# Performance work log

Measured on AMD Instinct MI355X. Metric: run time of the kernel, lower is better.

## Reference

```python
import jax, jax.numpy as jnp
import numpy as np

IN_F = 4096
OUT_F = 4096

def setup_inputs() -> dict:
    key = jax.random.key(0)
    k1, k2 = jax.random.split(key)
    x = jax.random.normal(k1, (8, 2048, IN_F), dtype=jnp.float32)
    weight = jax.random.normal(k2, (OUT_F, IN_F), dtype=jnp.float32) * (1.0 / IN_F ** 0.5)
    bias = jnp.zeros((OUT_F,), dtype=jnp.float32)
    return {"x": x, "weight": weight, "bias": bias}

def reference(x, weight, bias):
    # absmean scale over the full weight matrix (BitNet b1.58)
    scale = jnp.maximum(jnp.mean(jnp.abs(weight)), 1e-8)
    w_quant = jnp.clip(jnp.round(weight / scale), -1.0, 1.0)  # ternary {-1,0,+1}
    # straight-through estimator: forward uses w_quant*scale, grad flows to weight
    w_ste = jax.lax.stop_gradient(w_quant * scale - weight) + weight
    # x: [b, s, in], w_ste: [out, in] -> [b, s, out]
    return jnp.einsum('bsi,oi->bso', x, w_ste) + bias
```

## Files before the change

kernel.cpp:

```cpp
#include <hip/hip_runtime.h>
#include <stdint.h>
#include <stddef.h>

#define M_DIM 16384
#define K_DIM 4096
#define N_DIM 4096

#define BM 128
#define BN 128
#define BK 32

#define WS_SUM_OFF   0
#define WS_PART_OFF  256
#define WS_X_OFF     16384
#define WS_XBYTES    ((size_t)M_DIM * K_DIM * 2)
#define WS_W_OFF     (WS_X_OFF + WS_XBYTES)
#define WS_WBYTES    ((size_t)N_DIM * K_DIM * 2)
#define WS_NEEDED    (WS_W_OFF + WS_WBYTES)

typedef __attribute__((ext_vector_type(8))) short short8;
typedef __attribute__((ext_vector_type(4))) float floatx4;

__device__ __forceinline__ unsigned short f2bf_rne(float f) {
  unsigned u = __builtin_bit_cast(unsigned, f);
  u += 0x7FFFu + ((u >> 16) & 1u);
  return (unsigned short)(u >> 16);
}

__device__ __forceinline__ float get_scale(const double* __restrict__ sum) {
  double m = *sum * (1.0 / 16777216.0);
  return (float)fmax(m, 1e-8);
}

__device__ __forceinline__ void gload16(const void* g, void* l) {
  __builtin_amdgcn_global_load_lds(
      (const __attribute__((address_space(1))) void*)g,
      (__attribute__((address_space(3))) void*)l,
      16, 0, 0);
}

__global__ void prep_kernel(const float* __restrict__ W, double* __restrict__ partials,
                            const float* __restrict__ X, unsigned short* __restrict__ XO) {
  if (blockIdx.x < 1024) {
    const int n4 = (N_DIM * K_DIM) / 4;
    const float4* W4 = (const float4*)W;
    float s = 0.f;
    const int stride = 1024 * blockDim.x;
    for (int i = blockIdx.x * blockDim.x + threadIdx.x; i < n4; i += stride) {
      float4 v = W4[i];
      s += fabsf(v.x) + fabsf(v.y) + fabsf(v.z) + fabsf(v.w);
    }
#pragma unroll
    for (int off = 32; off > 0; off >>= 1) s += __shfl_down(s, off);
    __shared__ double bsum[4];
    if ((threadIdx.x & 63) == 0) bsum[threadIdx.x >> 6] = (double)s;
    __syncthreads();
    if (threadIdx.x == 0)
      partials[blockIdx.x] = bsum[0] + bsum[1] + bsum[2] + bsum[3];
  } else {
    const int n4 = (M_DIM * K_DIM) / 4;
    const float4* X4 = (const float4*)X;
    ushort4* O4 = (ushort4*)XO;
    const int nblk = 3072;
    const int stride = nblk * blockDim.x;
    for (int i = (blockIdx.x - 1024) * blockDim.x + threadIdx.x; i < n4; i += stride) {
      float4 v = X4[i];
      ushort4 o;
      o.x = f2bf_rne(v.x); o.y = f2bf_rne(v.y); o.z = f2bf_rne(v.z); o.w = f2bf_rne(v.w);
      O4[i] = o;
    }
  }
}

__global__ void reduce2_kernel(const double* __restrict__ partials, double* __restrict__ sum) {
  double s = 0.0;
  for (int i = threadIdx.x; i < 1024; i += 256) s += partials[i];
#pragma unroll
  for (int off = 32; off > 0; off >>= 1) s += __shfl_down(s, off);
  __shared__ double wsum[4];
  if ((threadIdx.x & 63) == 0) wsum[threadIdx.x >> 6] = s;
  __syncthreads();
  if (threadIdx.x == 0) *sum = wsum[0] + wsum[1] + wsum[2] + wsum[3];
}

__global__ void quantw_kernel(const float* __restrict__ W, const double* __restrict__ sum,
                              unsigned short* __restrict__ T) {
  const int n4 = (N_DIM * K_DIM) / 4;
  const float s = get_scale(sum);
  const float4* W4 = (const float4*)W;
  ushort4* T4 = (ushort4*)T;
  const int stride = gridDim.x * blockDim.x;
  for (int i = blockIdx.x * blockDim.x + threadIdx.x; i < n4; i += stride) {
    float4 v = W4[i];
    float q0 = fminf(fmaxf(rintf(v.x / s), -1.f), 1.f);
    float q1 = fminf(fmaxf(rintf(v.y / s), -1.f), 1.f);
    float q2 = fminf(fmaxf(rintf(v.z / s), -1.f), 1.f);
    float q3 = fminf(fmaxf(rintf(v.w / s), -1.f), 1.f);
    ushort4 o;
    o.x = f2bf_rne(q0); o.y = f2bf_rne(q1); o.z = f2bf_rne(q2); o.w = f2bf_rne(q3);
    T4[i] = o;
  }
}

__global__ __launch_bounds__(256) void gemm_kernel(
    const unsigned short* __restrict__ A,
    const unsigned short* __restrict__ B,
    const float* __restrict__ bias,
    const double* __restrict__ sum,
    float* __restrict__ C) {
  __shared__ __align__(16) unsigned short sA[BM * BK];
  __shared__ __align__(16) unsigned short sB[BN * BK];

  const int tid = threadIdx.x;
  const int w = tid >> 6;
  const int l = tid & 63;
  const int wm = w & 1;
  const int wn = w >> 1;
  const int blockM = blockIdx.y * BM;
  const int blockN = blockIdx.x * BN;

  const int srow = w * 16 + (l >> 2);
  const int skc = ((l & 3) ^ ((l >> 3) & 3)) * 8;
  const unsigned short* pA0 = A + (size_t)(blockM + srow) * K_DIM + skc;
  const unsigned short* pA1 = pA0 + (size_t)64 * K_DIM;
  const unsigned short* pB0 = B + (size_t)(blockN + srow) * K_DIM + skc;
  const unsigned short* pB1 = pB0 + (size_t)64 * K_DIM;
  char* ldsA0 = (char*)sA + w * 1024;
  char* ldsA1 = (char*)sA + 4096 + w * 1024;
  char* ldsB0 = (char*)sB + w * 1024;
  char* ldsB1 = (char*)sB + 4096 + w * 1024;

  const int arow = wm * 64 + (l & 15);
  const int brow = wn * 64 + (l & 15);
  const int koff = (((l >> 4) ^ ((l >> 1) & 3))) * 8;

  floatx4 acc[4][4] = {};

  for (int kt = 0; kt < K_DIM / BK; ++kt) {
    __syncthreads();
    gload16(pA0, ldsA0);
    gload16(pA1, ldsA1);
    gload16(pB0, ldsB0);
    gload16(pB1, ldsB1);
    pA0 += BK; pA1 += BK; pB0 += BK; pB1 += BK;
    __syncthreads();

    short8 af[4], bf[4];
#pragma unroll
    for (int mi = 0; mi < 4; ++mi)
      af[mi] = *(const short8*)&sA[(arow + mi * 16) * BK + koff];
#pragma unroll
    for (int ni = 0; ni < 4; ++ni)
      bf[ni] = *(const short8*)&sB[(brow + ni * 16) * BK + koff];
#pragma unroll
    for (int mi = 0; mi < 4; ++mi)
#pragma unroll
      for (int ni = 0; ni < 4; ++ni)
        acc[mi][ni] = __builtin_amdgcn_mfma_f32_16x16x32_bf16(
            af[mi], bf[ni], acc[mi][ni], 0, 0, 0);
  }

  const float s = get_scale(sum);
  const int col16 = l & 15;
  const int rquad = (l >> 4) * 4;
#pragma unroll
  for (int mi = 0; mi < 4; ++mi) {
#pragma unroll
    for (int ni = 0; ni < 4; ++ni) {
      const int col = blockN + wn * 64 + ni * 16 + col16;
      const float bv = bias[col];
      const int row0 = blockM + wm * 64 + mi * 16 + rquad;
#pragma unroll
      for (int r = 0; r < 4; ++r) {
        C[(size_t)(row0 + r) * N_DIM + col] = acc[mi][ni][r] * s + bv;
      }
    }
  }
}

extern "C" void kernel_launch(void* const* d_in, const int* in_sizes, int n_in,
                              void* d_out, int out_size, void* d_ws, size_t ws_size,
                              hipStream_t stream) {
  const float* x = (const float*)d_in[0];
  const float* wt = (const float*)d_in[1];
  const float* bias = (const float*)d_in[2];
  float* out = (float*)d_out;

  if (ws_size < WS_NEEDED) return;

  double* sum = (double*)((char*)d_ws + WS_SUM_OFF);
  double* partials = (double*)((char*)d_ws + WS_PART_OFF);
  unsigned short* xb = (unsigned short*)((char*)d_ws + WS_X_OFF);
  unsigned short* wb = (unsigned short*)((char*)d_ws + WS_W_OFF);

  prep_kernel<<<4096, 256, 0, stream>>>(wt, partials, x, xb);
  reduce2_kernel<<<1, 256, 0, stream>>>(partials, sum);
  quantw_kernel<<<1024, 256, 0, stream>>>(wt, sum, wb);
  dim3 grid(N_DIM / BN, M_DIM / BM);
  gemm_kernel<<<grid, 256, 0, stream>>>(xb, wb, bias, sum, out);
}
```

Measured before the change: 1.083 ms.

## Rewrite GEMM as 256x256x64 double-buffered pipelined kernel with interleaved staging

Replaces the 128x128x32 single-buffered GEMM with a 512-thread 256x256x64 tile kernel. Its 128KB LDS is split into two ping-pong buffers, and global-to-LDS loads for future k-tiles are interleaved between MFMA quads, using explicit barriers, waitcnt and setprio. It also remaps block IDs for L2 locality and changes the LDS XOR swizzle. The aim is to hide global load latency and raise arithmetic intensity per LDS byte, at the cost of heavy register and LDS use and fragile hand-tuned synchronization.

```diff
diff --git a/kernel.cpp b/kernel.cpp
--- a/kernel.cpp
+++ b/kernel.cpp
@@ -6,9 +6,9 @@
 #define K_DIM 4096
 #define N_DIM 4096
 
-#define BM 128
-#define BN 128
-#define BK 32
+#define BM 256
+#define BN 256
+#define BK 64
 
 #define WS_SUM_OFF   0
 #define WS_PART_OFF  256
@@ -102,78 +102,175 @@
   }
 }
 
-__global__ __launch_bounds__(256) void gemm_kernel(
+__device__ __forceinline__ void stage64(const unsigned short* __restrict__ src,
+                                        int gRow0, int kBase, char* ldsSlab) {
+  const int t = threadIdx.x;
+  const int r = t >> 3;
+  const int g = (t & 7) ^ (r & 7);
+  gload16(src + (size_t)(gRow0 + r) * K_DIM + kBase + (g << 3),
+          ldsSlab + ((t >> 6) << 10));
+}
+
+template <int Q>
+__device__ __forceinline__ void mfma_quad(floatx4 (&acc)[8][4],
+                                          const short8 (&F)[2][2],
+                                          const short8 (&bfr)[4][2]) {
+#pragma unroll
+  for (int j = 0; j < 2; ++j) {
+#pragma unroll
+    for (int ni = 0; ni < 4; ++ni) {
+      acc[2 * Q + j][ni] = __builtin_amdgcn_mfma_f32_16x16x32_bf16(
+          F[j][0], bfr[ni][0], acc[2 * Q + j][ni], 0, 0, 0);
+      acc[2 * Q + j][ni] = __builtin_amdgcn_mfma_f32_16x16x32_bf16(
+          F[j][1], bfr[ni][1], acc[2 * Q + j][ni], 0, 0, 0);
+    }
+  }
+}
+
+#define LDA(P, off) (*(const short8*)(smem + (P) * 65536 + (off)))
+#define LDB(P, off) (*(const short8*)(smem + (P) * 65536 + 32768 + (off)))
+
+#define TILE_BODY(T, P)                                                       \
+  {                                                                           \
+      \
+    _Pragma("unroll")                                                         \
+    for (int ni = 0; ni < 4; ++ni) {                                          \
+      bf[ni][0] = LDB(P, bOff0 + ni * 2048);                                  \
+      bf[ni][1] = LDB(P, bOff1 + ni * 2048);                                  \
+    }                                                                         \
+    afA[0][0] = LDA(P, aOff0);        afA[0][1] = LDA(P, aOff1);              \
+    afA[1][0] = LDA(P, aOff0 + 2048); afA[1][1] = LDA(P, aOff1 + 2048);       \
+    if ((T) + 1 < 64) {                                                       \
+      stage64(B, blockN + 128, ((T) + 1) << 6,                                \
+              smem + (1 - (P)) * 65536 + 32768 + 128 * 128);                  \
+      stage64(B, blockN + 192, ((T) + 1) << 6,                                \
+              smem + (1 - (P)) * 65536 + 32768 + 192 * 128);                  \
+    }                                                                         \
+    __builtin_amdgcn_s_barrier();                                             \
+    asm volatile("s_waitcnt lgkmcnt(0)" ::: "memory");                        \
+    __builtin_amdgcn_sched_barrier(0);                                        \
+    __builtin_amdgcn_s_setprio(1);                                            \
+    mfma_quad<0>(acc, afA, bf);                                               \
+    __builtin_amdgcn_s_setprio(0);                                            \
+    __builtin_amdgcn_s_barrier();                                             \
+                                                               \
+    afA[0][0] = LDA(P, aOff0 + 4096); afA[0][1] = LDA(P, aOff1 + 4096);       \
+    afA[1][0] = LDA(P, aOff0 + 6144); afA[1][1] = LDA(P, aOff1 + 6144);       \
+    if ((T) + 2 < 64) {                                                       \
+      stage64(B, blockN + 0,  ((T) + 2) << 6, smem + (P) * 65536 + 32768);    \
+      stage64(B, blockN + 64, ((T) + 2) << 6,                                 \
+              smem + (P) * 65536 + 32768 + 64 * 128);                         \
+    }                                                                         \
+    __builtin_amdgcn_s_barrier();                                             \
+    asm volatile("s_waitcnt lgkmcnt(0)" ::: "memory");                        \
+    __builtin_amdgcn_sched_barrier(0);                                        \
+    __builtin_amdgcn_s_setprio(1);                                            \
+    mfma_quad<1>(acc, afA, bf);                                               \
+    __builtin_amdgcn_s_setprio(0);                                            \
+    __builtin_amdgcn_s_barrier();                                             \
+             \
+    afA[0][0] = LDA(P, aOff0 + 8192);  afA[0][1] = LDA(P, aOff1 + 8192);      \
+    afA[1][0] = LDA(P, aOff0 + 10240); afA[1][1] = LDA(P, aOff1 + 10240);     \
+    afB[0][0] = LDA(P, aOff0 + 12288); afB[0][1] = LDA(P, aOff1 + 12288);     \
+    afB[1][0] = LDA(P, aOff0 + 14336); afB[1][1] = LDA(P, aOff1 + 14336);     \
+    if ((T) + 2 < 64) {                                                       \
+      stage64(A, blockM + 0,   ((T) + 2) << 6, smem + (P) * 65536);           \
+      stage64(A, blockM + 128, ((T) + 2) << 6,                                \
+              smem + (P) * 65536 + 128 * 128);                                \
+    }                                                                         \
+    __builtin_amdgcn_s_barrier();                                             \
+    asm volatile("s_waitcnt lgkmcnt(0)" ::: "memory");                        \
+    __builtin_amdgcn_sched_barrier(0);                                        \
+    __builtin_amdgcn_s_setprio(1);                                            \
+    mfma_quad<2>(acc, afA, bf);                                               \
+    __builtin_amdgcn_s_setprio(0);                                            \
+    __builtin_amdgcn_s_barrier();                                             \
+                        \
+    if ((T) + 2 < 64) {                                                       \
+      stage64(A, blockM + 64,  ((T) + 2) << 6,                                \
+              smem + (P) * 65536 + 64 * 128);                                 \
+      stage64(A, blockM + 192, ((T) + 2) << 6,                                \
+              smem + (P) * 65536 + 192 * 128);                                \
+    }                                                                         \
+    __builtin_amdgcn_s_barrier();                                             \
+    __builtin_amdgcn_s_setprio(1);                                            \
+    mfma_quad<3>(acc, afB, bf);                                               \
+    __builtin_amdgcn_s_setprio(0);                                            \
+    if ((T) < 62) {                                                           \
+      asm volatile("s_waitcnt vmcnt(6)" ::: "memory");                        \
+      __builtin_amdgcn_s_barrier();                                           \
+    } else if ((T) == 62) {                                                   \
+      asm volatile("s_waitcnt vmcnt(0)" ::: "memory");                        \
+      __builtin_amdgcn_s_barrier();                                           \
+    }                                                                         \
+  }
+
+__global__ __launch_bounds__(512, 2) void gemm_kernel(
     const unsigned short* __restrict__ A,
     const unsigned short* __restrict__ B,
     const float* __restrict__ bias,
     const double* __restrict__ sum,
     float* __restrict__ C) {
-  __shared__ __align__(16) unsigned short sA[BM * BK];
-  __shared__ __align__(16) unsigned short sB[BN * BK];
+  __shared__ __align__(16) char smem[131072];
 
   const int tid = threadIdx.x;
-  const int w = tid >> 6;
   const int l = tid & 63;
-  const int wm = w & 1;
-  const int wn = w >> 1;
-  const int blockM = blockIdx.y * BM;
-  const int blockN = blockIdx.x * BN;
-
-  const int srow = w * 16 + (l >> 2);
-  const int skc = ((l & 3) ^ ((l >> 3) & 3)) * 8;
-  const unsigned short* pA0 = A + (size_t)(blockM + srow) * K_DIM + skc;
-  const unsigned short* pA1 = pA0 + (size_t)64 * K_DIM;
-  const unsigned short* pB0 = B + (size_t)(blockN + srow) * K_DIM + skc;
-  const unsigned short* pB1 = pB0 + (size_t)64 * K_DIM;
-  char* ldsA0 = (char*)sA + w * 1024;
-  char* ldsA1 = (char*)sA + 4096 + w * 1024;
-  char* ldsB0 = (char*)sB + w * 1024;
-  char* ldsB1 = (char*)sB + 4096 + w * 1024;
-
-  const int arow = wm * 64 + (l & 15);
-  const int brow = wn * 64 + (l & 15);
-  const int koff = (((l >> 4) ^ ((l >> 1) & 3))) * 8;
-
-  floatx4 acc[4][4] = {};
-
-  for (int kt = 0; kt < K_DIM / BK; ++kt) {
-    __syncthreads();
-    gload16(pA0, ldsA0);
-    gload16(pA1, ldsA1);
-    gload16(pB0, ldsB0);
-    gload16(pB1, ldsB1);
-    pA0 += BK; pA1 += BK; pB0 += BK; pB1 += BK;
-    __syncthreads();
-
-    short8 af[4], bf[4];
-#pragma unroll
-    for (int mi = 0; mi < 4; ++mi)
-      af[mi] = *(const short8*)&sA[(arow + mi * 16) * BK + koff];
-#pragma unroll
-    for (int ni = 0; ni < 4; ++ni)
-      bf[ni] = *(const short8*)&sB[(brow + ni * 16) * BK + koff];
-#pragma unroll
-    for (int mi = 0; mi < 4; ++mi)
-#pragma unroll
-      for (int ni = 0; ni < 4; ++ni)
-        acc[mi][ni] = __builtin_amdgcn_mfma_f32_16x16x32_bf16(
-            af[mi], bf[ni], acc[mi][ni], 0, 0, 0);
+  const int wid = tid >> 6;
+  const int wm = wid >> 2;
+  const int wn = wid & 3;
+
+  const int lin = blockIdx.x;
+  const int swz = ((lin & 7) << 7) | (lin >> 3);
+  const int blockM = (swz >> 4) << 8;
+  const int blockN = (swz & 15) << 8;
+
+  const int laneRow = l & 15;
+  const int c0 = (l >> 4) ^ (l & 7);
+  const int aOff0 = ((wm * 128 + laneRow) * 8 + c0) << 4;
+  const int aOff1 = aOff0 ^ 64;
+  const int bOff0 = ((wn * 64 + laneRow) * 8 + c0) << 4;
+  const int bOff1 = bOff0 ^ 64;
+
+  floatx4 acc[8][4] = {};
+  short8 bf[4][2], afA[2][2], afB[2][2];
+
+  stage64(A, blockM + 0,   0, smem + 0);
+  stage64(A, blockM + 128, 0, smem + 128 * 128);
+  stage64(A, blockM + 64,  0, smem + 64 * 128);
+  stage64(A, blockM + 192, 0, smem + 192 * 128);
+  stage64(B, blockN + 0,   0, smem + 32768);
+  stage64(B, blockN + 64,  0, smem + 32768 + 64 * 128);
+  stage64(B, blockN + 128, 0, smem + 32768 + 128 * 128);
+  stage64(B, blockN + 192, 0, smem + 32768 + 192 * 128);
+  stage64(B, blockN + 0,   64, smem + 65536 + 32768);
+  stage64(B, blockN + 64,  64, smem + 65536 + 32768 + 64 * 128);
+  stage64(A, blockM + 0,   64, smem + 65536);
+  stage64(A, blockM + 128, 64, smem + 65536 + 128 * 128);
+  stage64(A, blockM + 64,  64, smem + 65536 + 64 * 128);
+  stage64(A, blockM + 192, 64, smem + 65536 + 192 * 128);
+  asm volatile("s_waitcnt vmcnt(6)" ::: "memory");
+  __builtin_amdgcn_s_barrier();
+
+  for (int tp = 0; tp < 32; ++tp) {
+    const int t0 = tp * 2;
+    TILE_BODY(t0, 0)
+    TILE_BODY(t0 + 1, 1)
   }
 
   const float s = get_scale(sum);
   const int col16 = l & 15;
   const int rquad = (l >> 4) * 4;
 #pragma unroll
-  for (int mi = 0; mi < 4; ++mi) {
-#pragma unroll
-    for (int ni = 0; ni < 4; ++ni) {
-      const int col = blockN + wn * 64 + ni * 16 + col16;
-      const float bv = bias[col];
-      const int row0 = blockM + wm * 64 + mi * 16 + rquad;
-#pragma unroll
-      for (int r = 0; r < 4; ++r) {
-        C[(size_t)(row0 + r) * N_DIM + col] = acc[mi][ni][r] * s + bv;
-      }
+  for (int ni = 0; ni < 4; ++ni) {
+    const int col = blockN + wn * 64 + ni * 16 + col16;
+    const float bv = bias[col];
+#pragma unroll
+    for (int mi = 0; mi < 8; ++mi) {
+      const int row0 = blockM + wm * 128 + mi * 16 + rquad;
+      float* Cp = C + (size_t)row0 * N_DIM + col;
+#pragma unroll
+      for (int r = 0; r < 4; ++r)
+        Cp[(size_t)r * N_DIM] = acc[mi][ni][r] * s + bv;
     }
   }
 }
@@ -196,6 +293,5 @@
   prep_kernel<<<4096, 256, 0, stream>>>(wt, partials, x, xb);
   reduce2_kernel<<<1, 256, 0, stream>>>(partials, sum);
   quantw_kernel<<<1024, 256, 0, stream>>>(wt, sum, wb);
-  dim3 grid(N_DIM / BN, M_DIM / BM);
-  gemm_kernel<<<grid, 256, 0, stream>>>(xb, wb, bias, sum, out);
-}
+  gemm_kernel<<<1024, 512, 0, stream>>>(xb, wb, bias, sum, out);
+}
```

New measurement: 898.0 us. -17.1%, faster.
